# Kernel optimization log

Measured on AMD Instinct MI355X. Metric: run time of the kernel, lower is better.

## Reference

```python
import jax, jax.numpy as jnp
import numpy as np

ORDER = 8
ALPHA = 1.0
BETA = 1.0
IN_SIZE = 512
OUT_SIZE = 512
BATCH = 4096


def jacobi_values(x, order, a, b):
    """x: [B, I] raw input. Returns Jacobi polynomial values [B, I, order+1]."""
    x = jnp.tanh(x)
    vals = [jnp.ones_like(x), 0.5 * (a + b + 2) * x - 0.5 * (a - b)]
    for i in range(2, order + 1):
        k1 = (2 * i + a + b) * (2 * i + a + b - 1) / (2 * i * (i + a + b))
        k2 = (2 * i + a + b - 1) * (a * a - b * b) / (2 * i * (i + a + b) * (2 * i + a + b - 2))
        k3 = (i + a - 1) * (i + b - 1) * (2 * i + a + b) / (i * (i + a + b) * (2 * i + a + b - 2))
        vals.append((k1 * x + k2) * vals[-1] - k3 * vals[-2])
    return jnp.stack(vals, axis=-1)


def setup_inputs() -> dict:
    key = jax.random.key(0)
    kx, kw, kc = jax.random.split(key, 3)
    x = jax.random.normal(kx, (BATCH, IN_SIZE), dtype=jnp.float32)
    weights = jax.random.normal(kw, (OUT_SIZE, IN_SIZE), dtype=jnp.float32)
    # coefficients: one (order+1)-vector per (output, input) pair, init ~ N(0,1)*0.1
    coeff = jax.random.normal(kc, (OUT_SIZE, IN_SIZE, ORDER + 1), dtype=jnp.float32) * 0.1
    return {"x": x, "weights": weights, "coeff": coeff}


def reference(x, weights, coeff):
    # J: [B, I, K] with K = order+1
    J = jacobi_values(x, ORDER, ALPHA, BETA)
    # transformed_x[b,o,i] = sum_k coeff[o,i,k] * J[b,i,k]
    # output[b,o] = sum_i transformed_x[b,o,i] * weights[o,i]
    return jnp.einsum('bik,oik,oi->bo', J, coeff, weights)
```

## Files before the change

### kernel.cpp

```cpp
#include <hip/hip_runtime.h>
#include <hip/hip_bf16.h>

constexpr int BATCH = 4096;
constexpr int IN    = 512;
constexpr int OUT   = 512;
constexpr int ORD   = 8;
constexpr int NK    = ORD + 1;
constexpr float FA  = 1.0f, FB = 1.0f;

constexpr int KP     = IN * ORD;
constexpr int SPLITK = 4;
constexpr int KT     = KP / (32 * SPLITK);
constexpr int KS_TOT = KP / 32;

typedef __attribute__((ext_vector_type(8))) short short8;
typedef __attribute__((ext_vector_type(4))) float floatx4;

#define AS1 __attribute__((address_space(1)))
#define AS3 __attribute__((address_space(3)))

__device__ __forceinline__ float bf16bits_to_f32(short s) {
    union { unsigned int u; float f; } cv;
    cv.u = ((unsigned int)(unsigned short)s) << 16;
    return cv.f;
}
__device__ __forceinline__ short f32_to_bf16bits(float f) {
    __hip_bfloat16 h = __float2bfloat16(f);
    return *(short*)&h;
}

__global__ __launch_bounds__(256) void prep(const float* __restrict__ x,
                                            const float* __restrict__ w,
                                            const float* __restrict__ coeff,
                                            short* __restrict__ A2,
                                            short* __restrict__ B2,
                                            float* __restrict__ bias) {
    const int bid  = blockIdx.x;
    const int tid  = threadIdx.x;
    const int lane = tid & 63;
    const int quad = lane >> 4;
    const int l15  = lane & 15;

    if (bid < 1024) {
        const int mt  = bid >> 2;
        const int sub = ((bid & 3) << 2) + (tid >> 6);
        const int b   = mt * 16 + l15;
        const int i0  = sub * 32 + quad * 8;
        const float* xr = x + (size_t)b * IN + i0;
        float t[8];
#pragma unroll
        for (int e = 0; e < 8; ++e) {
            float xc = fminf(fmaxf(xr[e], -9.0f), 9.0f);
            float ex = __expf(2.0f * xc);
            t[e] = (ex - 1.0f) / (ex + 1.0f);
        }
        float pp[8], pc[8];
#pragma unroll
        for (int e = 0; e < 8; ++e) {
            pp[e] = 1.0f;
            pc[e] = 0.5f * (FA + FB + 2.0f) * t[e] - 0.5f * (FA - FB);
        }
        {
            short8 v;
#pragma unroll
            for (int e = 0; e < 8; ++e) v[e] = f32_to_bf16bits(pc[e]);
            *(short8*)(A2 + (((size_t)mt * KS_TOT + sub) * 64 + lane) * 8) = v;
        }
#pragma unroll
        for (int n = 2; n <= ORD; ++n) {
            float fn = (float)n;
            float k1 = (2.f*fn+FA+FB)*(2.f*fn+FA+FB-1.f) / (2.f*fn*(fn+FA+FB));
            float k2 = (2.f*fn+FA+FB-1.f)*(FA*FA-FB*FB) /
                       (2.f*fn*(fn+FA+FB)*(2.f*fn+FA+FB-2.f));
            float k3 = (fn+FA-1.f)*(fn+FB-1.f)*(2.f*fn+FA+FB) /
                       (fn*(fn+FA+FB)*(2.f*fn+FA+FB-2.f));
            short8 v;
#pragma unroll
            for (int e = 0; e < 8; ++e) {
                float nx = (k1*t[e] + k2)*pc[e] - k3*pp[e];
                pp[e] = pc[e]; pc[e] = nx;
                v[e] = f32_to_bf16bits(nx);
            }
            const int ks = (n - 1) * 16 + sub;
            *(short8*)(A2 + (((size_t)mt * KS_TOT + ks) * 64 + lane) * 8) = v;
        }
    } else if (bid < 1152) {
        const int b2  = bid - 1024;
        const int nt  = b2 >> 2;
        const int sub = ((b2 & 3) << 2) + (tid >> 6);
        const int o   = nt * 16 + l15;
        const int i0  = sub * 32 + quad * 8;
        const float* wr = w + (size_t)o * IN + i0;
        float wv[8];
#pragma unroll
        for (int e = 0; e < 8; ++e) wv[e] = wr[e];
        const float* cf = coeff + ((size_t)o * IN + i0) * NK;
#pragma unroll
        for (int n = 1; n <= ORD; ++n) {
            short8 v;
#pragma unroll
            for (int e = 0; e < 8; ++e)
                v[e] = f32_to_bf16bits(cf[(size_t)e * NK + n] * wv[e]);
            const int ks = (n - 1) * 16 + sub;
            *(short8*)(B2 + (((size_t)nt * KS_TOT + ks) * 64 + lane) * 8) = v;
        }
    } else {
        const int bb = bid - 1152;
        const int o  = bb * 4 + (tid >> 6);
        const float* cf = coeff + (size_t)o * IN * NK;
        const float* wr = w + (size_t)o * IN;
        float acc = 0.0f;
#pragma unroll
        for (int r = 0; r < IN / 64; ++r) {
            int i = r * 64 + lane;
            acc = fmaf(cf[(size_t)i * NK], wr[i], acc);
        }
#pragma unroll
        for (int off = 32; off >= 1; off >>= 1)
            acc += __shfl_xor(acc, off, 64);
        if (lane == 0) bias[o] = acc;
    }
}

__global__ __launch_bounds__(256, 3) void gemm_splitk(
        const short* __restrict__ A2,
        const short* __restrict__ B2,
        __hip_bfloat16* __restrict__ P)
{
    __shared__ short sA[3 * 2 * 8 * 512];

    const int tid  = threadIdx.x;
    const int lane = tid & 63;
    const int quad = lane >> 4;
    const int l15  = lane & 15;
    const int wave = tid >> 6;
    const int mw   = wave & 1;
    const int nw   = wave >> 1;
    const int bx = blockIdx.x;
    const int by = blockIdx.y;
    const int z  = blockIdx.z;

    const short* pb[2];
#pragma unroll
    for (int j = 0; j < 2; ++j)
        pb[j] = B2 + (((size_t)(by * 4 + nw * 2 + j) * KS_TOT + z * KT) * 64 + lane) * 8;

    const int wv = wave;
    const short* aBase = A2 + ((size_t)(bx * 8) * KS_TOT + z * KT) * 512;

#define STAGE2(BT, BUF)                                                      \
    _Pragma("unroll")                                                        \
    for (int c = 0; c < 4; ++c) {                                            \
        const int ll = c * 4 + wv;                                           \
        const int mt = ll & 7;                                               \
        const int s  = ll >> 3;                                              \
        __builtin_amdgcn_global_load_lds(                                    \
            (const AS1 unsigned int*)(aBase +                                \
                ((size_t)mt * KS_TOT + (BT) * 2 + s) * 512 + lane * 8),      \
            (AS3 unsigned int*)(sA + (BUF) * 8192 + (c * 256 + tid) * 8),    \
            16, 0, 0);                                                       \
    }

#define BLOAD(S0, S1, K0)                                                    \
    _Pragma("unroll")                                                        \
    for (int j = 0; j < 2; ++j) {                                            \
        S0[j] = *(const short8*)(pb[j] + (K0) * 512);                        \
        S1[j] = *(const short8*)(pb[j] + ((K0) + 1) * 512);                  \
    }

    floatx4 acc[4][2];
#pragma unroll
    for (int i = 0; i < 4; ++i)
#pragma unroll
        for (int j = 0; j < 2; ++j) acc[i][j] = (floatx4)0.0f;

#define ASTEP(BUFI, S, BSLOT)                                                \
    {                                                                        \
        short8 af[4];                                                        \
        _Pragma("unroll")                                                    \
        for (int i = 0; i < 4; ++i)                                          \
            af[i] = *(const short8*)(sA + (BUFI) * 8192 +                    \
                        (((S) * 8 + mw * 4 + i) * 64 + lane) * 8);           \
        __builtin_amdgcn_s_setprio(1);                                       \
        _Pragma("unroll")                                                    \
        for (int i = 0; i < 4; ++i)                                          \
            _Pragma("unroll")                                                \
            for (int j = 0; j < 2; ++j)                                      \
                acc[i][j] = __builtin_amdgcn_mfma_f32_16x16x32_bf16(         \
                                af[i], BSLOT[j], acc[i][j], 0, 0, 0);        \
        __builtin_amdgcn_s_setprio(0);                                       \
    }

    short8 bsA0[2], bsA1[2], bsB0[2], bsB1[2];

    STAGE2(0, 0)
    STAGE2(1, 1)
    BLOAD(bsA0, bsA1, 0)
    asm volatile("s_waitcnt vmcnt(8)" ::: "memory");
    __builtin_amdgcn_s_barrier();

#pragma unroll
    for (int t = 0; t < 14; ++t) {
        if ((t & 1) == 0) { BLOAD(bsB0, bsB1, 2 * t + 2) }
        else              { BLOAD(bsA0, bsA1, 2 * t + 2) }
        STAGE2(t + 2, (t + 2) % 3)
        if ((t & 1) == 0) { ASTEP(t % 3, 0, bsA0) ASTEP(t % 3, 1, bsA1) }
        else              { ASTEP(t % 3, 0, bsB0) ASTEP(t % 3, 1, bsB1) }
        asm volatile("s_waitcnt vmcnt(8)" ::: "memory");
        __builtin_amdgcn_s_barrier();
    }
    BLOAD(bsB0, bsB1, 30)
    ASTEP(2, 0, bsA0) ASTEP(2, 1, bsA1)
    asm volatile("s_waitcnt vmcnt(4)" ::: "memory");
    __builtin_amdgcn_s_barrier();
    ASTEP(0, 0, bsB0) ASTEP(0, 1, bsB1)

#undef ASTEP
#undef BLOAD
#undef STAGE2

    __hip_bfloat16* Pz = P + (size_t)z * BATCH * OUT;
    const int m0 = bx * 128, n0 = by * 64;
#pragma unroll
    for (int i = 0; i < 4; ++i) {
        const int r0 = m0 + mw * 64 + i * 16 + quad * 4;
#pragma unroll
        for (int j = 0; j < 2; ++j) {
            const int c = n0 + nw * 32 + j * 16 + l15;
#pragma unroll
            for (int r = 0; r < 4; ++r)
                Pz[(size_t)(r0 + r) * OUT + c] = __float2bfloat16(acc[i][j][r]);
        }
    }
}

__global__ __launch_bounds__(256) void reducek(const short* __restrict__ P,
                                               const float* __restrict__ bias,
                                               float* __restrict__ out) {
    const int j = blockIdx.x * 256 + threadIdx.x;
    const size_t base = (size_t)j * 8;
    constexpr size_t PLANE = (size_t)BATCH * OUT;

    float s[8];
    {
        short8 v = *(const short8*)(P + base);
#pragma unroll
        for (int e = 0; e < 8; ++e) s[e] = bf16bits_to_f32(v[e]);
    }
#pragma unroll
    for (int z = 1; z < SPLITK; ++z) {
        short8 v = *(const short8*)(P + z * PLANE + base);
#pragma unroll
        for (int e = 0; e < 8; ++e) s[e] += bf16bits_to_f32(v[e]);
    }
    const int o0 = (int)(base & (OUT - 1));
    const floatx4 b0 = *(const floatx4*)(bias + o0);
    const floatx4 b1 = *(const floatx4*)(bias + o0 + 4);
    floatx4 r0 = {s[0] + b0[0], s[1] + b0[1], s[2] + b0[2], s[3] + b0[3]};
    floatx4 r1 = {s[4] + b1[0], s[5] + b1[1], s[6] + b1[2], s[7] + b1[3]};
    *(floatx4*)(out + base)     = r0;
    *(floatx4*)(out + base + 4) = r1;
}

extern "C" void kernel_launch(void* const* d_in, const int* in_sizes, int n_in,
                              void* d_out, int out_size, void* d_ws, size_t ws_size,
                              hipStream_t stream) {
    const float* x     = (const float*)d_in[0];
    const float* w     = (const float*)d_in[1];
    const float* coeff = (const float*)d_in[2];
    float* out = (float*)d_out;

    char* ws = (char*)d_ws;
    short* A2 = (short*)ws;
    char* p1c = ws + (size_t)BATCH * KP * 2;
    short* B2 = (short*)p1c;
    char* p2c = p1c + (size_t)OUT * KP * 2;
    __hip_bfloat16* P = (__hip_bfloat16*)p2c;
    float* bias = (float*)(p2c + (size_t)SPLITK * BATCH * OUT * 2);

    prep<<<1280, 256, 0, stream>>>(x, w, coeff, A2, B2, bias);
    gemm_splitk<<<dim3(32, 8, SPLITK), 256, 0, stream>>>(A2, B2, P);
    reducek<<<BATCH * OUT / 8 / 256, 256, 0, stream>>>((const short*)P, bias, out);
}
```

Measured before the change: 105.4 us.

## Drop split-K and fuse bias epilogue into full-K GEMM with 4-stage LDS ring

The GEMM now runs the full K dimension in each block instead of a 4-way split-K. It writes fp32 output plus bias directly, so the bf16 partial buffer and the separate reduction kernel go away. The A-tile LDS staging goes from three to four buffers, and the unrolled main loop is restructured to match. This removes 16 MB-scale partial traffic and one kernel launch, and avoids rounding the partials to bf16. The cost is a grid of 256 blocks at one wave per SIMD, which gives much less parallelism to hide memory latency.

```diff
diff --git a/kernel.cpp b/kernel.cpp
--- a/kernel.cpp
+++ b/kernel.cpp
@@ -9,8 +9,6 @@
 constexpr float FA  = 1.0f, FB = 1.0f;
 
 constexpr int KP     = IN * ORD;
-constexpr int SPLITK = 4;
-constexpr int KT     = KP / (32 * SPLITK);
 constexpr int KS_TOT = KP / 32;
 
 typedef __attribute__((ext_vector_type(8))) short short8;
@@ -122,12 +120,13 @@
     }
 }
 
-__global__ __launch_bounds__(256, 3) void gemm_splitk(
+__global__ __launch_bounds__(256) void gemm_full(
         const short* __restrict__ A2,
         const short* __restrict__ B2,
-        __hip_bfloat16* __restrict__ P)
+        const float* __restrict__ bias,
+        float* __restrict__ out)
 {
-    __shared__ short sA[3 * 2 * 8 * 512];
+    __shared__ short sA[4 * 8192];
 
     const int tid  = threadIdx.x;
     const int lane = tid & 63;
@@ -138,15 +137,14 @@
     const int nw   = wave >> 1;
     const int bx = blockIdx.x;
     const int by = blockIdx.y;
-    const int z  = blockIdx.z;
 
     const short* pb[2];
 #pragma unroll
     for (int j = 0; j < 2; ++j)
-        pb[j] = B2 + (((size_t)(by * 4 + nw * 2 + j) * KS_TOT + z * KT) * 64 + lane) * 8;
+        pb[j] = B2 + (((size_t)(by * 4 + nw * 2 + j) * KS_TOT) * 64 + lane) * 8;
 
     const int wv = wave;
-    const short* aBase = A2 + ((size_t)(bx * 8) * KS_TOT + z * KT) * 512;
+    const short* aBase = A2 + ((size_t)(bx * 8) * KS_TOT) * 512;
 
 #define STAGE2(BT, BUF)                                                      \
     _Pragma("unroll")                                                        \
@@ -164,8 +162,8 @@
 #define BLOAD(S0, S1, K0)                                                    \
     _Pragma("unroll")                                                        \
     for (int j = 0; j < 2; ++j) {                                            \
-        S0[j] = *(const short8*)(pb[j] + (K0) * 512);                        \
-        S1[j] = *(const short8*)(pb[j] + ((K0) + 1) * 512);                  \
+        S0[j] = *(const short8*)(pb[j] + (size_t)(K0) * 512);                \
+        S1[j] = *(const short8*)(pb[j] + (size_t)((K0) + 1) * 512);          \
     }
 
     floatx4 acc[4][2];
@@ -194,33 +192,46 @@
     short8 bsA0[2], bsA1[2], bsB0[2], bsB1[2];
 
     STAGE2(0, 0)
+    BLOAD(bsA0, bsA1, 0)
     STAGE2(1, 1)
-    BLOAD(bsA0, bsA1, 0)
+    STAGE2(2, 2)
+    asm volatile("s_waitcnt vmcnt(12)" ::: "memory");
+    __builtin_amdgcn_s_barrier();
+
+#define ITERX(T, BUFI, SBUF, C0, C1, L0, L1)                                 \
+    BLOAD(L0, L1, 2 * (T) + 2)                                               \
+    STAGE2((T) + 3, SBUF)                                                    \
+    ASTEP(BUFI, 0, C0) ASTEP(BUFI, 1, C1)                                    \
+    asm volatile("s_waitcnt vmcnt(12)" ::: "memory");                        \
+    __builtin_amdgcn_s_barrier();
+
+    for (int q = 0; q < 15; ++q) {
+        const int t0 = q * 4;
+        ITERX(t0,     0, 3, bsA0, bsA1, bsB0, bsB1)
+        ITERX(t0 + 1, 1, 0, bsB0, bsB1, bsA0, bsA1)
+        ITERX(t0 + 2, 2, 1, bsA0, bsA1, bsB0, bsB1)
+        ITERX(t0 + 3, 3, 2, bsB0, bsB1, bsA0, bsA1)
+    }
+    ITERX(60, 0, 3, bsA0, bsA1, bsB0, bsB1)
+    BLOAD(bsA0, bsA1, 124)
+    ASTEP(1, 0, bsB0) ASTEP(1, 1, bsB1)
     asm volatile("s_waitcnt vmcnt(8)" ::: "memory");
     __builtin_amdgcn_s_barrier();
-
-#pragma unroll
-    for (int t = 0; t < 14; ++t) {
-        if ((t & 1) == 0) { BLOAD(bsB0, bsB1, 2 * t + 2) }
-        else              { BLOAD(bsA0, bsA1, 2 * t + 2) }
-        STAGE2(t + 2, (t + 2) % 3)
-        if ((t & 1) == 0) { ASTEP(t % 3, 0, bsA0) ASTEP(t % 3, 1, bsA1) }
-        else              { ASTEP(t % 3, 0, bsB0) ASTEP(t % 3, 1, bsB1) }
-        asm volatile("s_waitcnt vmcnt(8)" ::: "memory");
-        __builtin_amdgcn_s_barrier();
-    }
-    BLOAD(bsB0, bsB1, 30)
+    BLOAD(bsB0, bsB1, 126)
     ASTEP(2, 0, bsA0) ASTEP(2, 1, bsA1)
     asm volatile("s_waitcnt vmcnt(4)" ::: "memory");
     __builtin_amdgcn_s_barrier();
-    ASTEP(0, 0, bsB0) ASTEP(0, 1, bsB1)
-
+    ASTEP(3, 0, bsB0) ASTEP(3, 1, bsB1)
+
+#undef ITERX
 #undef ASTEP
 #undef BLOAD
 #undef STAGE2
 
-    __hip_bfloat16* Pz = P + (size_t)z * BATCH * OUT;
     const int m0 = bx * 128, n0 = by * 64;
+    float bj[2];
+#pragma unroll
+    for (int j = 0; j < 2; ++j) bj[j] = bias[n0 + nw * 32 + j * 16 + l15];
 #pragma unroll
     for (int i = 0; i < 4; ++i) {
         const int r0 = m0 + mw * 64 + i * 16 + quad * 4;
@@ -229,37 +240,9 @@
             const int c = n0 + nw * 32 + j * 16 + l15;
 #pragma unroll
             for (int r = 0; r < 4; ++r)
-                Pz[(size_t)(r0 + r) * OUT + c] = __float2bfloat16(acc[i][j][r]);
-        }
-    }
-}
-
-__global__ __launch_bounds__(256) void reducek(const short* __restrict__ P,
-                                               const float* __restrict__ bias,
-                                               float* __restrict__ out) {
-    const int j = blockIdx.x * 256 + threadIdx.x;
-    const size_t base = (size_t)j * 8;
-    constexpr size_t PLANE = (size_t)BATCH * OUT;
-
-    float s[8];
-    {
-        short8 v = *(const short8*)(P + base);
-#pragma unroll
-        for (int e = 0; e < 8; ++e) s[e] = bf16bits_to_f32(v[e]);
-    }
-#pragma unroll
-    for (int z = 1; z < SPLITK; ++z) {
-        short8 v = *(const short8*)(P + z * PLANE + base);
-#pragma unroll
-        for (int e = 0; e < 8; ++e) s[e] += bf16bits_to_f32(v[e]);
-    }
-    const int o0 = (int)(base & (OUT - 1));
-    const floatx4 b0 = *(const floatx4*)(bias + o0);
-    const floatx4 b1 = *(const floatx4*)(bias + o0 + 4);
-    floatx4 r0 = {s[0] + b0[0], s[1] + b0[1], s[2] + b0[2], s[3] + b0[3]};
-    floatx4 r1 = {s[4] + b1[0], s[5] + b1[1], s[6] + b1[2], s[7] + b1[3]};
-    *(floatx4*)(out + base)     = r0;
-    *(floatx4*)(out + base + 4) = r1;
+                out[(size_t)(r0 + r) * OUT + c] = acc[i][j][r] + bj[j];
+        }
+    }
 }
 
 extern "C" void kernel_launch(void* const* d_in, const int* in_sizes, int n_in,
@@ -274,11 +257,8 @@
     short* A2 = (short*)ws;
     char* p1c = ws + (size_t)BATCH * KP * 2;
     short* B2 = (short*)p1c;
-    char* p2c = p1c + (size_t)OUT * KP * 2;
-    __hip_bfloat16* P = (__hip_bfloat16*)p2c;
-    float* bias = (float*)(p2c + (size_t)SPLITK * BATCH * OUT * 2);
+    float* bias = (float*)(p1c + (size_t)OUT * KP * 2);
 
     prep<<<1280, 256, 0, stream>>>(x, w, coeff, A2, B2, bias);
-    gemm_splitk<<<dim3(32, 8, SPLITK), 256, 0, stream>>>(A2, B2, P);
-    reducek<<<BATCH * OUT / 8 / 256, 256, 0, stream>>>((const short*)P, bias, out);
-}
+    gemm_full<<<dim3(32, 8), 256, 0, stream>>>(A2, B2, bias, out);
+}
```

Result: slower. 111.6 us (+5.9%).
